# Kernel optimization log

Measured on AMD Instinct MI355X. Metric: run time of the kernel, lower is better.

## Reference

```python
import jax, jax.numpy as jnp
import numpy as np

B, N, C, H, W, NH, SR = 16, 4096, 128, 64, 64, 4, 8
LN_EPS = 1e-5


def _conv(x, w, b, stride, padding, groups=1):
    y = jax.lax.conv_general_dilated(
        x, w, (stride, stride), padding,
        feature_group_count=groups,
        dimension_numbers=('NCHW', 'OIHW', 'NCHW'))
    return y + b[None, :, None, None]


def _layernorm(x, g, b):
    m = jnp.mean(x, axis=-1, keepdims=True)
    v = jnp.mean((x - m) ** 2, axis=-1, keepdims=True)
    return (x - m) / jnp.sqrt(v + LN_EPS) * g + b


def setup_inputs() -> dict:
    key = jax.random.key(0)
    ks = jax.random.split(key, 12)
    s = 0.02
    return {
        'x': jax.random.normal(ks[0], (B, N, C), jnp.float32),
        'q_w': jax.random.normal(ks[1], (C, C), jnp.float32) * s,
        'sr1_w': jax.random.normal(ks[2], (C, C, SR, SR), jnp.float32) * s,
        'sr1_b': jnp.zeros((C,), jnp.float32),
        'n1_g': jnp.ones((C,), jnp.float32),
        'n1_b': jnp.zeros((C,), jnp.float32),
        'sr2_w': jax.random.normal(ks[3], (C, C, SR // 2, SR // 2), jnp.float32) * s,
        'sr2_b': jnp.zeros((C,), jnp.float32),
        'n2_g': jnp.ones((C,), jnp.float32),
        'n2_b': jnp.zeros((C,), jnp.float32),
        'kv1_w': jax.random.normal(ks[4], (C, C), jnp.float32) * s,
        'kv2_w': jax.random.normal(ks[5], (C, C), jnp.float32) * s,
        'lc1_w': jax.random.normal(ks[6], (C // 2, 1, 3, 3), jnp.float32) * s,
        'lc1_b': jnp.zeros((C // 2,), jnp.float32),
        'lc2_w': jax.random.normal(ks[7], (C // 2, 1, 3, 3), jnp.float32) * s,
        'lc2_b': jnp.zeros((C // 2,), jnp.float32),
        'proj_w': jax.random.normal(ks[8], (C, C), jnp.float32) * s,
        'proj_b': jnp.zeros((C,), jnp.float32),
        'h': H,
        'w': W,
    }


def _forward(x, q_w, sr1_w, sr1_b, n1_g, n1_b, sr2_w, sr2_b, n2_g, n2_b,
             kv1_w, kv2_w, lc1_w, lc1_b, lc2_w, lc2_b, proj_w, proj_b, h, w):
    b, n, c = x.shape
    nh, sr = NH, SR
    hh = nh // 2          # heads per branch
    d = c // nh           # head dim
    scale = d ** -0.5

    q = (x @ q_w.T).reshape(b, n, nh, d).transpose(0, 2, 1, 3)  # (b,nh,n,d)
    x_img = x.transpose(0, 2, 1).reshape(b, c, h, w)

    def branch(sr_w, sr_b, g, beta, kv_w, lc_w, lc_b, stride, q_part):
        hp, wp = h // stride, w // stride
        m = hp * wp
        t = _conv(x_img, sr_w, sr_b, stride, 'VALID')          # (b,c,hp,wp)
        t = t.reshape(b, c, m).transpose(0, 2, 1)              # (b,m,c)
        t = jax.nn.gelu(_layernorm(t, g, beta), approximate=False)
        kv = (t @ kv_w.T).reshape(b, m, 2, hh, d).transpose(2, 0, 3, 1, 4)
        k, v = kv[0], kv[1]                                    # (b,hh,m,d)
        attn = jax.nn.softmax(
            jnp.einsum('bhnd,bhmd->bhnm', q_part, k) * scale, axis=-1)
        # local depthwise conv on v over the reduced spatial grid
        v_img = v.transpose(0, 2, 1, 3).reshape(b, m, c // 2)
        v_img = v_img.transpose(0, 2, 1).reshape(b, c // 2, hp, wp)
        v_loc = _conv(v_img, lc_w, lc_b, 1, [(1, 1), (1, 1)], groups=c // 2)
        v = v + v_loc.reshape(b, hh, d, m).transpose(0, 1, 3, 2)
        out = jnp.einsum('bhnm,bhmd->bhnd', attn, v)           # (b,hh,n,d)
        return out.transpose(0, 2, 1, 3).reshape(b, n, c // 2)

    x1 = branch(sr1_w, sr1_b, n1_g, n1_b, kv1_w, lc1_w, lc1_b, sr, q[:, :hh])
    x2 = branch(sr2_w, sr2_b, n2_g, n2_b, kv2_w, lc2_w, lc2_b, sr // 2, q[:, hh:])
    return jnp.concatenate([x1, x2], axis=-1) @ proj_w.T + proj_b


def reference(x, q_w, sr1_w, sr1_b, n1_g, n1_b, sr2_w, sr2_b, n2_g, n2_b,
              kv1_w, kv2_w, lc1_w, lc1_b, lc2_w, lc2_b, proj_w, proj_b, h, w):
    return _forward(x, q_w, sr1_w, sr1_b, n1_g, n1_b, sr2_w, sr2_b, n2_g, n2_b,
                    kv1_w, kv2_w, lc1_w, lc1_b, lc2_w, lc2_b, proj_w, proj_b, h, w)
```

## Files before the change

kernel.cpp:

```cpp
#include <hip/hip_runtime.h>
#include <math.h>

#define B_ 16
#define N_ 4096

typedef __attribute__((ext_vector_type(8))) short short8v;
typedef __attribute__((ext_vector_type(4))) short short4v;
typedef __attribute__((ext_vector_type(4))) float f32x4;

__device__ __forceinline__ unsigned short f2bf(float f) {
  unsigned int u = __float_as_uint(f);
  return (unsigned short)((u + 0x7FFFu + ((u >> 16) & 1u)) >> 16);
}

__device__ __forceinline__ unsigned int pk2(float a, float b) {
  return (unsigned int)f2bf(a) | ((unsigned int)f2bf(b) << 16);
}

__device__ __forceinline__ short8v cvt8f(const float* p) {
  float4 a = *reinterpret_cast<const float4*>(p);
  float4 b = *reinterpret_cast<const float4*>(p + 4);
  short8v r;
  r[0] = (short)f2bf(a.x); r[1] = (short)f2bf(a.y);
  r[2] = (short)f2bf(a.z); r[3] = (short)f2bf(a.w);
  r[4] = (short)f2bf(b.x); r[5] = (short)f2bf(b.y);
  r[6] = (short)f2bf(b.z); r[7] = (short)f2bf(b.w);
  return r;
}

__global__ __launch_bounds__(256) void prep(const float* __restrict__ x,
    unsigned short* __restrict__ xT, const float* __restrict__ a,
    const float* __restrict__ b, const float* __restrict__ c,
    const float* __restrict__ d, const float* __restrict__ s1,
    const float* __restrict__ s2, unsigned short* __restrict__ wa,
    unsigned short* __restrict__ wb, unsigned short* __restrict__ wc,
    unsigned short* __restrict__ wd, unsigned short* __restrict__ w1,
    unsigned short* __restrict__ w2) {
  __shared__ float lds[32 * 132];
  const int t = threadIdx.x;
  if (blockIdx.x < 2048) {
    const int bb = blockIdx.x >> 7, pt = blockIdx.x & 127;
    const int ptile = pt * 32;
    for (int i = t; i < 1024; i += 256) {
      int p = i >> 5, c4 = (i & 31) << 2;
      *reinterpret_cast<float4*>(&lds[p * 132 + c4]) =
          *reinterpret_cast<const float4*>(
              x + ((size_t)(bb * 4096 + ptile + p)) * 128 + c4);
    }
    __syncthreads();
    const int ch = t >> 1, p0 = (t & 1) * 16;
    unsigned short* dst = xT + (size_t)bb * 524288 + ch * 4096 + ptile + p0;
    uint4 u0, u1;
    u0.x = pk2(lds[(p0 + 0) * 132 + ch], lds[(p0 + 1) * 132 + ch]);
    u0.y = pk2(lds[(p0 + 2) * 132 + ch], lds[(p0 + 3) * 132 + ch]);
    u0.z = pk2(lds[(p0 + 4) * 132 + ch], lds[(p0 + 5) * 132 + ch]);
    u0.w = pk2(lds[(p0 + 6) * 132 + ch], lds[(p0 + 7) * 132 + ch]);
    u1.x = pk2(lds[(p0 + 8) * 132 + ch], lds[(p0 + 9) * 132 + ch]);
    u1.y = pk2(lds[(p0 + 10) * 132 + ch], lds[(p0 + 11) * 132 + ch]);
    u1.z = pk2(lds[(p0 + 12) * 132 + ch], lds[(p0 + 13) * 132 + ch]);
    u1.w = pk2(lds[(p0 + 14) * 132 + ch], lds[(p0 + 15) * 132 + ch]);
    *reinterpret_cast<uint4*>(dst) = u0;
    *reinterpret_cast<uint4*>(dst + 8) = u1;
  } else {
    int i = (blockIdx.x - 2048) * 256 + t;
    if (i < 16384) wa[i] = f2bf(a[i]);
    else if (i < 32768) { int o = i - 16384; wb[o] = f2bf(b[o]); }
    else if (i < 49152) { int o = i - 32768; wc[o] = f2bf(c[o]); }
    else if (i < 65536) { int o = i - 49152; wd[o] = f2bf(d[o]); }
    else if (i < 65536 + 1048576) { int o = i - 65536; w1[o] = f2bf(s1[o]); }
    else { int o = i - 65536 - 1048576; w2[o] = f2bf(s2[o]); }
  }
}

template <int SRV, int KSP>
__device__ void conv_body(int bx, int by, const unsigned short* __restrict__ xT,
    const unsigned short* __restrict__ W, float* __restrict__ part) {
  constexpr int WP = 64 / SRV;
  constexpr int M = WP * WP;
  constexpr int ROWS = B_ * M;
  constexpr int SS = SRV * SRV;
  constexpr int KTOT = 128 * SS;
  constexpr int LSS = (SRV == 8) ? 6 : 4;
  constexpr int LM = (SRV == 8) ? 6 : 8;
  constexpr int LWP = (SRV == 8) ? 3 : 4;
  const int t = threadIdx.x;
  const int wid = t >> 6, lane = t & 63;
  const int lrow = lane & 15, lk = (lane >> 4) << 3;
  const int r0 = bx * 128 + wid * 32;
  const int kb0 = by * KSP;
  int rbase[2], pixoff[2];
#pragma unroll
  for (int m = 0; m < 2; m++) {
    int row = r0 + m * 16 + lrow;
    int b = row >> LM, p = row & (M - 1);
    int ph = p >> LWP, pw = p & (WP - 1);
    rbase[m] = b << 19;
    pixoff[m] = (ph * SRV) * 64 + pw * SRV;
  }
  f32x4 acc[2][8];
#pragma unroll
  for (int m = 0; m < 2; m++)
#pragma unroll
    for (int n = 0; n < 8; n++) acc[m][n] = (f32x4)(0.f);
  for (int k0 = 0; k0 < KSP; k0 += 32) {
    int k = kb0 + k0 + lk;
    int ci = k >> LSS;
    int rem = k & (SS - 1);
    short8v a[2], bf[8];
#pragma unroll
    for (int m = 0; m < 2; m++) {
      if constexpr (SRV == 8) {
        a[m] = *reinterpret_cast<const short8v*>(
            xT + (size_t)rbase[m] + ci * 4096 + pixoff[m] + (rem >> 3) * 64);
      } else {
        int kh0 = rem >> 2;
        short4v lo = *reinterpret_cast<const short4v*>(
            xT + (size_t)rbase[m] + ci * 4096 + pixoff[m] + kh0 * 64);
        short4v hi = *reinterpret_cast<const short4v*>(
            xT + (size_t)rbase[m] + ci * 4096 + pixoff[m] + (kh0 + 1) * 64);
        short8v av;
        av[0] = lo[0]; av[1] = lo[1]; av[2] = lo[2]; av[3] = lo[3];
        av[4] = hi[0]; av[5] = hi[1]; av[6] = hi[2]; av[7] = hi[3];
        a[m] = av;
      }
    }
#pragma unroll
    for (int n = 0; n < 8; n++)
      bf[n] = *reinterpret_cast<const short8v*>(
          W + (size_t)(n * 16 + lrow) * KTOT + k);
#pragma unroll
    for (int m = 0; m < 2; m++)
#pragma unroll
      for (int n = 0; n < 8; n++)
        acc[m][n] = __builtin_amdgcn_mfma_f32_16x16x32_bf16(a[m], bf[n],
                                                            acc[m][n], 0, 0, 0);
  }
  const int rr = (lane >> 4) << 2;
#pragma unroll
  for (int m = 0; m < 2; m++)
#pragma unroll
    for (int n = 0; n < 8; n++) {
      int cc = n * 16 + lrow;
#pragma unroll
      for (int j = 0; j < 4; j++)
        part[((size_t)by * ROWS + r0 + m * 16 + rr + j) * 128 + cc] =
            acc[m][n][j];
    }
}

template <bool A_BF16, bool OUT_BF16, bool HAS_BIAS>
__device__ void gemm_body(int bx, const void* __restrict__ Araw,
    const unsigned short* __restrict__ W, const float* __restrict__ bias,
    void* __restrict__ out) {
  const int t = threadIdx.x;
  const int wid = t >> 6, lane = t & 63;
  const int lrow = lane & 15, lk = (lane >> 4) << 3;
  const int r0 = bx * 128 + wid * 32;
  f32x4 acc[2][8];
#pragma unroll
  for (int m = 0; m < 2; m++)
#pragma unroll
    for (int n = 0; n < 8; n++) acc[m][n] = (f32x4)(0.f);
#pragma unroll
  for (int k0 = 0; k0 < 128; k0 += 32) {
    short8v a[2], bf[8];
#pragma unroll
    for (int m = 0; m < 2; m++) {
      if constexpr (A_BF16)
        a[m] = *reinterpret_cast<const short8v*>(
            (const unsigned short*)Araw + (size_t)(r0 + m * 16 + lrow) * 128 +
            k0 + lk);
      else
        a[m] = cvt8f((const float*)Araw + (size_t)(r0 + m * 16 + lrow) * 128 +
                     k0 + lk);
    }
#pragma unroll
    for (int n = 0; n < 8; n++)
      bf[n] = *reinterpret_cast<const short8v*>(
          W + (size_t)(n * 16 + lrow) * 128 + k0 + lk);
#pragma unroll
    for (int m = 0; m < 2; m++)
#pragma unroll
      for (int n = 0; n < 8; n++)
        acc[m][n] = __builtin_amdgcn_mfma_f32_16x16x32_bf16(a[m], bf[n],
                                                            acc[m][n], 0, 0, 0);
  }
  const int rr = (lane >> 4) << 2;
#pragma unroll
  for (int m = 0; m < 2; m++)
#pragma unroll
    for (int n = 0; n < 8; n++) {
      int cc = n * 16 + lrow;
      float bv = HAS_BIAS ? bias[cc] : 0.f;
#pragma unroll
      for (int j = 0; j < 4; j++) {
        size_t idx = (size_t)(r0 + m * 16 + rr + j) * 128 + cc;
        float v = acc[m][n][j] + bv;
        if constexpr (OUT_BF16)
          ((unsigned short*)out)[idx] = f2bf(v);
        else
          ((float*)out)[idx] = v;
      }
    }
}

__global__ __launch_bounds__(256) void conv_q(
    const unsigned short* __restrict__ xT, const unsigned short* __restrict__ w1b,
    const unsigned short* __restrict__ w2b, float* __restrict__ part1,
    float* __restrict__ part2, const float* __restrict__ x,
    const unsigned short* __restrict__ wq, unsigned short* __restrict__ qb) {
  const int bid = blockIdx.x;
  if (bid < 256) {
    conv_body<8, 256>(bid & 7, bid >> 3, xT, w1b, part1);
  } else if (bid < 512) {
    int j = bid - 256;
    conv_body<4, 256>(j & 31, j >> 5, xT, w2b, part2);
  } else {
    gemm_body<false, true, false>(bid - 512, x, wq, nullptr, qb);
  }
}

__global__ __launch_bounds__(128) void ln_all(const float* __restrict__ part1,
    const float* __restrict__ part2, const float* __restrict__ cb1,
    const float* __restrict__ g1, const float* __restrict__ be1,
    const float* __restrict__ cb2, const float* __restrict__ g2,
    const float* __restrict__ be2, unsigned short* __restrict__ out1,
    unsigned short* __restrict__ out2) {
  const int t = threadIdx.x;
  int row = blockIdx.x;
  const float* part; const float *cb, *g, *be; unsigned short* out;
  int nsplit, rows;
  if (row < 1024) {
    part = part1; cb = cb1; g = g1; be = be1; out = out1;
    nsplit = 32; rows = 1024;
  } else {
    row -= 1024;
    part = part2; cb = cb2; g = g2; be = be2; out = out2;
    nsplit = 8; rows = 4096;
  }
  float v = cb[t];
  for (int s = 0; s < nsplit; s++)
    v += part[((size_t)s * rows + row) * 128 + t];
  float sv = v, sq = v * v;
#pragma unroll
  for (int off = 32; off > 0; off >>= 1) {
    sv += __shfl_down(sv, off, 64);
    sq += __shfl_down(sq, off, 64);
  }
  __shared__ float red0[2], red1[2];
  if ((t & 63) == 0) {
    red0[t >> 6] = sv;
    red1[t >> 6] = sq;
  }
  __syncthreads();
  float mean = (red0[0] + red0[1]) * (1.f / 128.f);
  float var = (red1[0] + red1[1]) * (1.f / 128.f) - mean * mean;
  float y = (v - mean) * rsqrtf(var + 1e-5f) * g[t] + be[t];
  out[(size_t)row * 128 + t] = f2bf(y * 0.5f * (1.f + erff(y * 0.70710678118f)));
}

__device__ void kv_body(int bx, const unsigned short* __restrict__ A,
    const unsigned short* __restrict__ W, unsigned short* __restrict__ kb,
    float* __restrict__ vr) {
  const int t = threadIdx.x;
  const int wid = t >> 6, lane = t & 63;
  const int lrow = lane & 15, lk = (lane >> 4) << 3;
  const int r0 = bx * 128 + wid * 32;
  f32x4 acc[2][8];
#pragma unroll
  for (int m = 0; m < 2; m++)
#pragma unroll
    for (int n = 0; n < 8; n++) acc[m][n] = (f32x4)(0.f);
#pragma unroll
  for (int k0 = 0; k0 < 128; k0 += 32) {
    short8v a[2], bf[8];
#pragma unroll
    for (int m = 0; m < 2; m++)
      a[m] = *reinterpret_cast<const short8v*>(
          A + (size_t)(r0 + m * 16 + lrow) * 128 + k0 + lk);
#pragma unroll
    for (int n = 0; n < 8; n++)
      bf[n] = *reinterpret_cast<const short8v*>(
          W + (size_t)(n * 16 + lrow) * 128 + k0 + lk);
#pragma unroll
    for (int m = 0; m < 2; m++)
#pragma unroll
      for (int n = 0; n < 8; n++)
        acc[m][n] = __builtin_amdgcn_mfma_f32_16x16x32_bf16(a[m], bf[n],
                                                            acc[m][n], 0, 0, 0);
  }
  const int rr = (lane >> 4) << 2;
#pragma unroll
  for (int m = 0; m < 2; m++)
#pragma unroll
    for (int n = 0; n < 8; n++) {
      int cc = n * 16 + lrow;
#pragma unroll
      for (int j = 0; j < 4; j++) {
        int r = r0 + m * 16 + rr + j;
        float v = acc[m][n][j];
        if (cc < 64)
          kb[(size_t)r * 64 + cc] = f2bf(v);
        else
          vr[(size_t)r * 64 + (cc - 64)] = v;
      }
    }
}

__global__ __launch_bounds__(256) void kv_all(
    const unsigned short* __restrict__ t1b, const unsigned short* __restrict__ wkv1,
    unsigned short* __restrict__ kb1, float* __restrict__ vr1,
    const unsigned short* __restrict__ t2b, const unsigned short* __restrict__ wkv2,
    unsigned short* __restrict__ kb2, float* __restrict__ vr2) {
  if (blockIdx.x < 8)
    kv_body(blockIdx.x, t1b, wkv1, kb1, vr1);
  else
    kv_body(blockIdx.x - 8, t2b, wkv2, kb2, vr2);
}

template <int WP>
__device__ void dw_body(int idx, const float* __restrict__ vr,
    const float* __restrict__ lw, const float* __restrict__ lb,
    float* __restrict__ vp) {
  constexpr int M = WP * WP;
  constexpr int LM = (WP == 8) ? 6 : 8;
  constexpr int LWPc = (WP == 8) ? 3 : 4;
  int ch = idx & 63;
  int rest = idx >> 6;
  int m = rest & (M - 1);
  int bb = rest >> LM;
  int y = m >> LWPc, x0 = m & (WP - 1);
  float s = lb[ch];
#pragma unroll
  for (int ky = 0; ky < 3; ky++) {
    int yy = y + ky - 1;
    if (yy < 0 || yy >= WP) continue;
#pragma unroll
    for (int kx = 0; kx < 3; kx++) {
      int xx = x0 + kx - 1;
      if (xx < 0 || xx >= WP) continue;
      s += vr[((size_t)(bb * M + yy * WP + xx)) * 64 + ch] *
           lw[ch * 9 + ky * 3 + kx];
    }
  }
  vp[idx] = vr[((size_t)(bb * M + m)) * 64 + ch] + s;
}

__global__ __launch_bounds__(256) void dw_all(const float* __restrict__ vr1,
    const float* __restrict__ lw1, const float* __restrict__ lb1,
    float* __restrict__ v1p, const float* __restrict__ vr2,
    const float* __restrict__ lw2, const float* __restrict__ lb2,
    float* __restrict__ v2p) {
  if (blockIdx.x < 256)
    dw_body<8>(blockIdx.x * 256 + threadIdx.x, vr1, lw1, lb1, v1p);
  else
    dw_body<16>((blockIdx.x - 256) * 256 + threadIdx.x, vr2, lw2, lb2, v2p);
}

template <int M>
__device__ void tv_body(int blk, const float* __restrict__ vp,
    unsigned short* __restrict__ vT, float* lds) {
  constexpr int TPB = M / 32;
  const int t = threadIdx.x;
  const int b = blk / TPB, mt = blk % TPB;
  const int m0 = mt * 32;
  for (int i = t; i < 512; i += 256) {
    int m = i >> 4, c4 = (i & 15) << 2;
    *reinterpret_cast<float4*>(&lds[m * 68 + c4]) =
        *reinterpret_cast<const float4*>(vp + ((size_t)(b * M + m0 + m)) * 64 + c4);
  }
  __syncthreads();
  const int c = t >> 2, ms = (t & 3) * 8;
  unsigned short* dst = vT + ((size_t)b * 64 + c) * M + m0 + ms;
  uint4 u;
  u.x = pk2(lds[(ms + 0) * 68 + c], lds[(ms + 1) * 68 + c]);
  u.y = pk2(lds[(ms + 2) * 68 + c], lds[(ms + 3) * 68 + c]);
  u.z = pk2(lds[(ms + 4) * 68 + c], lds[(ms + 5) * 68 + c]);
  u.w = pk2(lds[(ms + 6) * 68 + c], lds[(ms + 7) * 68 + c]);
  *reinterpret_cast<uint4*>(dst) = u;
}

__global__ __launch_bounds__(256) void tv_all(const float* __restrict__ v1p,
    unsigned short* __restrict__ vT1, const float* __restrict__ v2p,
    unsigned short* __restrict__ vT2) {
  __shared__ float lds[32 * 68];
  if (blockIdx.x < 32)
    tv_body<64>(blockIdx.x, v1p, vT1, lds);
  else
    tv_body<256>(blockIdx.x - 32, v2p, vT2, lds);
}

template <int M, int QOFF>
__device__ void attn_head(int b, int q0, int h,
    const unsigned short* __restrict__ qb, const unsigned short* Ks,
    const unsigned short* __restrict__ vT, unsigned short* __restrict__ xc,
    unsigned short* Plw) {
  constexpr int HM = (M > 128) ? 128 : M;
  constexpr int NCH = M / HM;
  constexpr int PSTR = HM + 8;
  constexpr int MT = M / 16;
  constexpr int HKS = HM / 32;
  const int lane = threadIdx.x & 63;
  const int lrow = lane & 15, g = lane >> 4;
  const int lk = g * 8;
  const size_t qrow = ((size_t)b * 4096 + q0 + lrow) * 128;
  const int qoff = QOFF + h * 32;
  const float scale = 0.17677669529663687f;
  short8v qf = *reinterpret_cast<const short8v*>(qb + qrow + qoff + lk);
  f32x4 s[MT];
#pragma unroll
  for (int mt = 0; mt < MT; mt++) {
    short8v kf = *reinterpret_cast<const short8v*>(
        Ks + (mt * 16 + lrow) * 72 + h * 32 + lk);
    s[mt] =
        __builtin_amdgcn_mfma_f32_16x16x32_bf16(kf, qf, (f32x4)(0.f), 0, 0, 0);
  }
  float l = 0.f;
#pragma unroll
  for (int mt = 0; mt < MT; mt++)
#pragma unroll
    for (int j = 0; j < 4; j++) {
      float p = __expf(s[mt][j] * scale);
      s[mt][j] = p;
      l += p;
    }
  l += __shfl_xor(l, 16, 64);
  l += __shfl_xor(l, 32, 64);
  f32x4 o[2];
  o[0] = (f32x4)(0.f);
  o[1] = (f32x4)(0.f);
#pragma unroll
  for (int half = 0; half < NCH; half++) {
#pragma unroll
    for (int mt2 = 0; mt2 < HM / 16; mt2++) {
      int mt = half * (HM / 16) + mt2;
      uint2 pw;
      pw.x = pk2(s[mt][0], s[mt][1]);
      pw.y = pk2(s[mt][2], s[mt][3]);
      *reinterpret_cast<uint2*>(&Plw[lrow * PSTR + mt2 * 16 + 4 * g]) = pw;
    }
    f32x4 oh[2];
    oh[0] = (f32x4)(0.f);
    oh[1] = (f32x4)(0.f);
#pragma unroll
    for (int ks = 0; ks < HKS; ks++) {
      short8v pf = *reinterpret_cast<const short8v*>(
          &Plw[lrow * PSTR + ks * 32 + lk]);
#pragma unroll
      for (int dt = 0; dt < 2; dt++) {
        short8v vf = *reinterpret_cast<const short8v*>(
            vT + ((size_t)b * 64 + h * 32 + dt * 16 + lrow) * M + half * HM +
            ks * 32 + lk);
        oh[dt] =
            __builtin_amdgcn_mfma_f32_16x16x32_bf16(vf, pf, oh[dt], 0, 0, 0);
      }
    }
#pragma unroll
    for (int dt = 0; dt < 2; dt++) o[dt] += oh[dt];
  }
  float linv = 1.f / l;
  unsigned short* orow = xc + qrow + qoff;
#pragma unroll
  for (int dt = 0; dt < 2; dt++) {
    uint2 u;
    u.x = pk2(o[dt][0] * linv, o[dt][1] * linv);
    u.y = pk2(o[dt][2] * linv, o[dt][3] * linv);
    *reinterpret_cast<uint2*>(orow + dt * 16 + 4 * g) = u;
  }
}

__global__ __launch_bounds__(256) void attn_all(
    const unsigned short* __restrict__ qb, const unsigned short* __restrict__ kb1,
    const unsigned short* __restrict__ vT1, const unsigned short* __restrict__ kb2,
    const unsigned short* __restrict__ vT2, unsigned short* __restrict__ xc) {
  __shared__ unsigned short Ks2[256 * 72];
  __shared__ unsigned short Ks1[64 * 72];
  __shared__ unsigned short Pl[4 * 16 * 136];
  const int t = threadIdx.x;
  const int b = blockIdx.x >> 6, qt = blockIdx.x & 63;
  for (int i = t; i < 2048; i += 256) {
    int row = i >> 3, seg = i & 7;
    *reinterpret_cast<uint4*>(&Ks2[row * 72 + seg * 8]) =
        *reinterpret_cast<const uint4*>(kb2 + ((size_t)b * 256 + row) * 64 +
                                        seg * 8);
  }
  for (int i = t; i < 512; i += 256) {
    int row = i >> 3, seg = i & 7;
    *reinterpret_cast<uint4*>(&Ks1[row * 72 + seg * 8]) =
        *reinterpret_cast<const uint4*>(kb1 + ((size_t)b * 64 + row) * 64 +
                                        seg * 8);
  }
  __syncthreads();
  const int wid = t >> 6;
  unsigned short* Plw = Pl + wid * 16 * 136;
  const int q0 = qt * 64 + wid * 16;
  attn_head<256, 64>(b, q0, 0, qb, Ks2, vT2, xc, Plw);
  attn_head<256, 64>(b, q0, 1, qb, Ks2, vT2, xc, Plw);
  attn_head<64, 0>(b, q0, 0, qb, Ks1, vT1, xc, Plw);
  attn_head<64, 0>(b, q0, 1, qb, Ks1, vT1, xc, Plw);
}

__global__ __launch_bounds__(256) void proj(const unsigned short* __restrict__ A,
    const unsigned short* __restrict__ W, const float* __restrict__ bias,
    float* __restrict__ out) {
  gemm_body<true, false, true>(blockIdx.x, A, W, bias, out);
}

extern "C" void kernel_launch(void* const* d_in, const int* in_sizes, int n_in,
                              void* d_out, int out_size, void* d_ws,
                              size_t ws_size, hipStream_t stream) {
  (void)in_sizes; (void)n_in; (void)out_size; (void)ws_size;
  const float* x      = (const float*)d_in[0];
  const float* q_w    = (const float*)d_in[1];
  const float* sr1_w  = (const float*)d_in[2];
  const float* sr1_b  = (const float*)d_in[3];
  const float* n1_g   = (const float*)d_in[4];
  const float* n1_b   = (const float*)d_in[5];
  const float* sr2_w  = (const float*)d_in[6];
  const float* sr2_b  = (const float*)d_in[7];
  const float* n2_g   = (const float*)d_in[8];
  const float* n2_b   = (const float*)d_in[9];
  const float* kv1_w  = (const float*)d_in[10];
  const float* kv2_w  = (const float*)d_in[11];
  const float* lc1_w  = (const float*)d_in[12];
  const float* lc1_b  = (const float*)d_in[13];
  const float* lc2_w  = (const float*)d_in[14];
  const float* lc2_b  = (const float*)d_in[15];
  const float* proj_w = (const float*)d_in[16];
  const float* proj_b = (const float*)d_in[17];

  char* w = (char*)d_ws;
  unsigned short* wq    = (unsigned short*)(w);
  unsigned short* wkv1  = (unsigned short*)(w + 32768);
  unsigned short* wkv2  = (unsigned short*)(w + 65536);
  unsigned short* wproj = (unsigned short*)(w + 98304);
  unsigned short* w1b   = (unsigned short*)(w + 131072);
  unsigned short* w2b   = (unsigned short*)(w + 2228224);
  unsigned short* xT  = (unsigned short*)(w + 2752512);
  unsigned short* qb  = (unsigned short*)(w + 2752512);
  unsigned short* kb1 = (unsigned short*)(w + 19529728);
  unsigned short* kb2 = (unsigned short*)(w + 19660800);
  float* part1 = (float*)(w + 33685504);
  float* part2 = (float*)(w + 33685504 + 16777216);
  unsigned short* xcb = (unsigned short*)(w + 33685504);
  unsigned short* t1b = (unsigned short*)(w + 69468160);
  unsigned short* t2b = (unsigned short*)(w + 69730304);
  float* vr1 = (float*)(w + 70778880);
  float* vr2 = (float*)(w + 71041024);
  float* v1p = (float*)(w + 72089600);
  float* v2p = (float*)(w + 72351744);
  unsigned short* vT1 = (unsigned short*)(w + 73400320);
  unsigned short* vT2 = (unsigned short*)(w + 73531392);

  prep<<<7424, 256, 0, stream>>>(x, xT, q_w, kv1_w, kv2_w, proj_w, sr1_w, sr2_w,
                                 wq, wkv1, wkv2, wproj, w1b, w2b);
  conv_q<<<1024, 256, 0, stream>>>(xT, w1b, w2b, part1, part2, x, wq, qb);
  ln_all<<<5120, 128, 0, stream>>>(part1, part2, sr1_b, n1_g, n1_b, sr2_b, n2_g,
                                   n2_b, t1b, t2b);
  kv_all<<<40, 256, 0, stream>>>(t1b, wkv1, kb1, vr1, t2b, wkv2, kb2, vr2);
  dw_all<<<1280, 256, 0, stream>>>(vr1, lc1_w, lc1_b, v1p, vr2, lc2_w, lc2_b, v2p);
  tv_all<<<160, 256, 0, stream>>>(v1p, vT1, v2p, vT2);
  attn_all<<<1024, 256, 0, stream>>>(qb, kb1, vT1, kb2, vT2, xcb);
  proj<<<512, 256, 0, stream>>>(xcb, wproj, proj_b, (float*)d_out);
}
```

Before: 124.2 us.

## Enlarge conv split-K chunks and feed Q GEMM from bf16 copy of x

```diff
diff --git a/kernel.cpp b/kernel.cpp
--- a/kernel.cpp
+++ b/kernel.cpp
@@ -29,13 +29,13 @@
 }
 
 __global__ __launch_bounds__(256) void prep(const float* __restrict__ x,
-    unsigned short* __restrict__ xT, const float* __restrict__ a,
-    const float* __restrict__ b, const float* __restrict__ c,
-    const float* __restrict__ d, const float* __restrict__ s1,
-    const float* __restrict__ s2, unsigned short* __restrict__ wa,
-    unsigned short* __restrict__ wb, unsigned short* __restrict__ wc,
-    unsigned short* __restrict__ wd, unsigned short* __restrict__ w1,
-    unsigned short* __restrict__ w2) {
+    unsigned short* __restrict__ xT, unsigned short* __restrict__ xb,
+    const float* __restrict__ a, const float* __restrict__ b,
+    const float* __restrict__ c, const float* __restrict__ d,
+    const float* __restrict__ s1, const float* __restrict__ s2,
+    unsigned short* __restrict__ wa, unsigned short* __restrict__ wb,
+    unsigned short* __restrict__ wc, unsigned short* __restrict__ wd,
+    unsigned short* __restrict__ w1, unsigned short* __restrict__ w2) {
   __shared__ float lds[32 * 132];
   const int t = threadIdx.x;
   if (blockIdx.x < 2048) {
@@ -48,6 +48,15 @@
               x + ((size_t)(bb * 4096 + ptile + p)) * 128 + c4);
     }
     __syncthreads();
+    for (int i = t; i < 1024; i += 256) {
+      int p = i >> 5, c4 = (i & 31) << 2;
+      const float* s = &lds[p * 132 + c4];
+      uint2 u;
+      u.x = pk2(s[0], s[1]);
+      u.y = pk2(s[2], s[3]);
+      *reinterpret_cast<uint2*>(
+          xb + ((size_t)(bb * 4096 + ptile + p)) * 128 + c4) = u;
+    }
     const int ch = t >> 1, p0 = (t & 1) * 16;
     unsigned short* dst = xT + (size_t)bb * 524288 + ch * 4096 + ptile + p0;
     uint4 u0, u1;
@@ -207,16 +216,16 @@
 __global__ __launch_bounds__(256) void conv_q(
     const unsigned short* __restrict__ xT, const unsigned short* __restrict__ w1b,
     const unsigned short* __restrict__ w2b, float* __restrict__ part1,
-    float* __restrict__ part2, const float* __restrict__ x,
-    const unsigned short* __restrict__ wq, unsigned short* __restrict__ qb) {
+    float* __restrict__ part2, unsigned short* __restrict__ xb,
+    const unsigned short* __restrict__ wq) {
   const int bid = blockIdx.x;
-  if (bid < 256) {
-    conv_body<8, 256>(bid & 7, bid >> 3, xT, w1b, part1);
-  } else if (bid < 512) {
-    int j = bid - 256;
-    conv_body<4, 256>(j & 31, j >> 5, xT, w2b, part2);
+  if (bid < 64) {
+    conv_body<8, 1024>(bid & 7, bid >> 3, xT, w1b, part1);
+  } else if (bid < 128) {
+    int j = bid - 64;
+    conv_body<4, 1024>(j & 31, j >> 5, xT, w2b, part2);
   } else {
-    gemm_body<false, true, false>(bid - 512, x, wq, nullptr, qb);
+    gemm_body<true, true, false>(bid - 128, xb, wq, nullptr, xb);
   }
 }
 
@@ -232,11 +241,11 @@
   int nsplit, rows;
   if (row < 1024) {
     part = part1; cb = cb1; g = g1; be = be1; out = out1;
-    nsplit = 32; rows = 1024;
+    nsplit = 8; rows = 1024;
   } else {
     row -= 1024;
     part = part2; cb = cb2; g = g2; be = be2; out = out2;
-    nsplit = 8; rows = 4096;
+    nsplit = 2; rows = 4096;
   }
   float v = cb[t];
   for (int s = 0; s < nsplit; s++)
@@ -537,12 +546,13 @@
   unsigned short* w1b   = (unsigned short*)(w + 131072);
   unsigned short* w2b   = (unsigned short*)(w + 2228224);
   unsigned short* xT  = (unsigned short*)(w + 2752512);
-  unsigned short* qb  = (unsigned short*)(w + 2752512);
   unsigned short* kb1 = (unsigned short*)(w + 19529728);
   unsigned short* kb2 = (unsigned short*)(w + 19660800);
   float* part1 = (float*)(w + 33685504);
-  float* part2 = (float*)(w + 33685504 + 16777216);
+  float* part2 = (float*)(w + 37879808);
   unsigned short* xcb = (unsigned short*)(w + 33685504);
+  unsigned short* xb  = (unsigned short*)(w + 50462720);
+  unsigned short* qb  = xb;
   unsigned short* t1b = (unsigned short*)(w + 69468160);
   unsigned short* t2b = (unsigned short*)(w + 69730304);
   float* vr1 = (float*)(w + 70778880);
@@ -552,9 +562,9 @@
   unsigned short* vT1 = (unsigned short*)(w + 73400320);
   unsigned short* vT2 = (unsigned short*)(w + 73531392);
 
-  prep<<<7424, 256, 0, stream>>>(x, xT, q_w, kv1_w, kv2_w, proj_w, sr1_w, sr2_w,
-                                 wq, wkv1, wkv2, wproj, w1b, w2b);
-  conv_q<<<1024, 256, 0, stream>>>(xT, w1b, w2b, part1, part2, x, wq, qb);
+  prep<<<7424, 256, 0, stream>>>(x, xT, xb, q_w, kv1_w, kv2_w, proj_w, sr1_w,
+                                 sr2_w, wq, wkv1, wkv2, wproj, w1b, w2b);
+  conv_q<<<640, 256, 0, stream>>>(xT, w1b, w2b, part1, part2, xb, wq);
   ln_all<<<5120, 128, 0, stream>>>(part1, part2, sr1_b, n1_g, n1_b, sr2_b, n2_g,
                                    n2_b, t1b, t2b);
   kv_all<<<40, 256, 0, stream>>>(t1b, wkv1, kb1, vr1, t2b, wkv2, kb2, vr2);
```

Result: slower. 128.6 us (+3.5%).
